# Kernel tuning notes

Hardware: AMD Instinct MI355X
Metric: run time of the kernel (lower is better)

The kernel has to match this reference:

```python
import jax, jax.numpy as jnp
import numpy as np

BN_EPS = 1e-3


def _three_nn(unknown, known):
    # unknown: [B, N2, 3] query points; known: [B, N1, 3]
    # returns squared distances and indices of the 3 nearest known points
    # (CUDA three_nn returns squared euclidean distances).
    d2 = (jnp.sum(unknown * unknown, -1)[:, :, None]
          + jnp.sum(known * known, -1)[:, None, :]
          - 2.0 * jnp.einsum('bnd,bmd->bnm', unknown, known))  # [B, N2, N1]
    neg_top, ind = jax.lax.top_k(-d2, 3)                        # [B, N2, 3]
    dist2 = jnp.maximum(-neg_top, 0.0)
    return dist2, ind


def _conv_bn_relu(x, W, b, gamma, beta, mean, var):
    # x: [B, C_in, N]; W: [C_out, C_in] (1x1 conv); inference-mode BN
    y = jnp.einsum('oc,bcn->bon', W, x) + b[None, :, None]
    scale = gamma / jnp.sqrt(var + BN_EPS)
    y = (y - mean[None, :, None]) * scale[None, :, None] + beta[None, :, None]
    return jax.nn.relu(y)


def setup_inputs() -> dict:
    key = jax.random.key(0)
    ks = jax.random.split(key, 12)
    B, N1, N2, C1, C2, H = 2, 4096, 16384, 256, 128, 256
    return {
        'points1': jax.random.normal(ks[0], (B, 3, N1), jnp.float32),
        'points2': jax.random.normal(ks[1], (B, 3, N2), jnp.float32),
        'features1': jax.random.normal(ks[2], (B, C1, N1), jnp.float32),
        'features2': jax.random.normal(ks[3], (B, C2, N2), jnp.float32),
        'W1': jax.random.normal(ks[4], (H, C1 + C2), jnp.float32) * 0.05,
        'b1': jax.random.normal(ks[5], (H,), jnp.float32) * 0.05,
        'gamma1': jnp.ones((H,), jnp.float32),
        'beta1': jnp.zeros((H,), jnp.float32),
        'mean1': jax.random.normal(ks[6], (H,), jnp.float32) * 0.1,
        'var1': jax.random.uniform(ks[7], (H,), jnp.float32, 0.5, 1.5),
        'W2': jax.random.normal(ks[8], (H, H), jnp.float32) * 0.05,
        'b2': jax.random.normal(ks[9], (H,), jnp.float32) * 0.05,
        'gamma2': jnp.ones((H,), jnp.float32),
        'beta2': jnp.zeros((H,), jnp.float32),
        'mean2': jax.random.normal(ks[10], (H,), jnp.float32) * 0.1,
        'var2': jax.random.uniform(ks[11], (H,), jnp.float32, 0.5, 1.5),
    }


def reference(points1, points2, features1, features2,
              W1, b1, gamma1, beta1, mean1, var1,
              W2, b2, gamma2, beta2, mean2, var2):
    # 3-NN of each dense point (points2) among coarse points (points1)
    unknown = jnp.swapaxes(points2, 1, 2)  # [B, N2, 3]
    known = jnp.swapaxes(points1, 1, 2)    # [B, N1, 3]
    dist, ind = _three_nn(unknown, known)  # dist: squared distances [B, N2, 3]
    dist = dist * dist                     # forward squares again (as in source)
    dist = jnp.maximum(dist, 1e-10)
    inv = 1.0 / dist
    weights = inv / jnp.sum(inv, axis=2, keepdims=True)  # [B, N2, 3]

    # gather features of the 3 neighbors: features1 [B, C1, N1] -> [B, N2, 3, C1]
    f1 = jnp.swapaxes(features1, 1, 2)  # [B, N1, C1]
    gathered = jax.vmap(lambda f, i: f[i])(f1, ind)  # [B, N2, 3, C1]
    interp = jnp.einsum('bnkc,bnk->bcn', gathered, weights)  # [B, C1, N2]

    x = jnp.concatenate([interp, features2], axis=1)  # [B, C1+C2, N2]
    x = _conv_bn_relu(x, W1, b1, gamma1, beta1, mean1, var1)
    x = _conv_bn_relu(x, W2, b2, gamma2, beta2, mean2, var2)
    return x
```

## Files before the change

### kernel.cpp

```cpp
#include <hip/hip_runtime.h>
#include <cstdint>
#include <cstddef>

#define N1 4096
#define N2 16384
#define C1 256
#define C2 128
#define HH 256
#define K1 384
#define BQ 32768
#define KPAD 392
#define NCH 8

typedef float  f32x4  __attribute__((ext_vector_type(4)));
typedef __bf16 bf16x8 __attribute__((ext_vector_type(8)));
typedef __bf16 bf16x4 __attribute__((ext_vector_type(4)));

__device__ __forceinline__ float exact_dd(float ux, float uy, float uz,
                                          float su, float4 p) {
  float dot = __fadd_rn(__fadd_rn(__fmul_rn(ux, p.x), __fmul_rn(uy, p.y)),
                        __fmul_rn(uz, p.z));
  return __builtin_fmaf(dot, -2.0f, __fadd_rn(su, p.w));
}

#define LEXINS(da, db, dc, ia, ib, ic, dd, jj)                                 \
  {                                                                            \
    bool ca = ((dd) < (da)) || ((dd) == (da) && (jj) < (ia));                  \
    bool cb = ((dd) < (db)) || ((dd) == (db) && (jj) < (ib));                  \
    bool cc = ((dd) < (dc)) || ((dd) == (dc) && (jj) < (ic));                  \
    dc = cb ? (db) : (cc ? (dd) : (dc));                                       \
    ic = cb ? (ib) : (cc ? (jj) : (ic));                                       \
    db = ca ? (da) : (cb ? (dd) : (db));                                       \
    ib = ca ? (ia) : (cb ? (jj) : (ib));                                       \
    da = ca ? (dd) : (da);                                                     \
    ia = ca ? (jj) : (ia);                                                     \
  }

#define KMIN4(K1_, K2_, K3_, K4_, x)                                           \
  {                                                                            \
    float n1 = fminf((K1_), (x));                                              \
    float n2 = __builtin_amdgcn_fmed3f((K1_), (x), (K2_));                     \
    float n3 = __builtin_amdgcn_fmed3f((K2_), (x), (K3_));                     \
    float n4 = __builtin_amdgcn_fmed3f((K3_), (x), (K4_));                     \
    K1_ = n1; K2_ = n2; K3_ = n3; K4_ = n4;                                    \
  }

#define POINTQ(ux, uy, uz, su, px, py, pz, pw, jj, Ka, Kb, Kc, Kd)             \
  {                                                                            \
    float dot_ = __fadd_rn(                                                    \
        __fadd_rn(__fmul_rn((ux), (px)), __fmul_rn((uy), (py))),               \
        __fmul_rn((uz), (pz)));                                                \
    float dd_ = __builtin_fmaf(dot_, -2.0f, __fadd_rn((su), (pw)));            \
    float xk_ = __uint_as_float((__float_as_uint(dd_) & 0xFFFFF000u) |         \
                                ((unsigned)(jj) & 0x00000FFFu));               \
    KMIN4(Ka, Kb, Kc, Kd, xk_);                                                \
  }

__global__ __launch_bounds__(256) void k_prep(
    const float* __restrict__ p1,
    const float* __restrict__ W1, const float* __restrict__ W2,
    const float* __restrict__ b1, const float* __restrict__ g1,
    const float* __restrict__ be1, const float* __restrict__ mm1,
    const float* __restrict__ vv1,
    const float* __restrict__ b2, const float* __restrict__ g2,
    const float* __restrict__ be2, const float* __restrict__ mm2,
    const float* __restrict__ vv2,
    float4* __restrict__ pts4,
    __bf16* __restrict__ W1b, __bf16* __restrict__ W2b,
    float* __restrict__ scsh) {
  int idx = blockIdx.x * 256 + threadIdx.x;
  if (idx < HH * K1) W1b[idx] = (__bf16)W1[idx];
  if (idx < HH * HH) W2b[idx] = (__bf16)W2[idx];
  if (idx < 2 * N1) {
    int b = idx >> 12, j = idx & (N1 - 1);
    const float* p = p1 + (size_t)b * 3 * N1;
    float x = p[j], y = p[N1 + j], z = p[2 * N1 + j];
    float sk = __fadd_rn(__fadd_rn(__fmul_rn(x, x), __fmul_rn(y, y)),
                         __fmul_rn(z, z));
    pts4[idx] = make_float4(x, y, z, sk);
  }
  if (idx < HH) {
    float sc = g1[idx] / sqrtf(vv1[idx] + 1e-3f);
    scsh[idx]          = sc;
    scsh[HH + idx]     = fmaf(b1[idx] - mm1[idx], sc, be1[idx]);
    float s2 = g2[idx] / sqrtf(vv2[idx] + 1e-3f);
    scsh[2 * HH + idx] = s2;
    scsh[3 * HH + idx] = fmaf(b2[idx] - mm2[idx], s2, be2[idx]);
  }
}

__global__ __launch_bounds__(256) void k_nn(
    const float* __restrict__ p2, const float4* __restrict__ pts4,
    float* __restrict__ keybuf) {
#pragma clang fp contract(off)
  __shared__ float4 spts[512];
  const int bx = blockIdx.x;
  const int ch = bx & (NCH - 1);
  const int qt = bx >> 3;
  const int b  = qt >> 5;
  const int nA = ((qt & 31) << 9) + threadIdx.x;
  const int nB = nA + 256;

  {
    const float4* g = pts4 + (size_t)b * N1 + ch * 512;
    spts[threadIdx.x]       = g[threadIdx.x];
    spts[threadIdx.x + 256] = g[threadIdx.x + 256];
  }

  const float* p2b = p2 + (size_t)b * 3 * N2;
  float uxA = p2b[nA], uyA = p2b[N2 + nA], uzA = p2b[2 * N2 + nA];
  float suA = __fadd_rn(__fadd_rn(__fmul_rn(uxA, uxA), __fmul_rn(uyA, uyA)),
                        __fmul_rn(uzA, uzA));
  float uxB = p2b[nB], uyB = p2b[N2 + nB], uzB = p2b[2 * N2 + nB];
  float suB = __fadd_rn(__fadd_rn(__fmul_rn(uxB, uxB), __fmul_rn(uyB, uyB)),
                        __fmul_rn(uzB, uzB));
  __syncthreads();

  const int j0 = ch * 512;
  float KaA = 3.0e38f, KbA = 3.0e38f, KcA = 3.0e38f, KdA = 3.0e38f;
  float KaB = 3.0e38f, KbB = 3.0e38f, KcB = 3.0e38f, KdB = 3.0e38f;
#pragma unroll 4
  for (int k = 0; k < 256; ++k) {
    float4 p0 = spts[2 * k];
    float4 p1 = spts[2 * k + 1];
    int i0 = j0 + 2 * k;
    int i1 = j0 + 2 * k + 1;
    POINTQ(uxA, uyA, uzA, suA, p0.x, p0.y, p0.z, p0.w, i0, KaA, KbA, KcA, KdA);
    POINTQ(uxA, uyA, uzA, suA, p1.x, p1.y, p1.z, p1.w, i1, KaA, KbA, KcA, KdA);
    POINTQ(uxB, uyB, uzB, suB, p0.x, p0.y, p0.z, p0.w, i0, KaB, KbB, KcB, KdB);
    POINTQ(uxB, uyB, uzB, suB, p1.x, p1.y, p1.z, p1.w, i1, KaB, KbB, KcB, KdB);
  }

  int qA = b * N2 + nA;
  int qB = b * N2 + nB;
  keybuf[(ch * 4 + 0) * BQ + qA] = KaA;
  keybuf[(ch * 4 + 1) * BQ + qA] = KbA;
  keybuf[(ch * 4 + 2) * BQ + qA] = KcA;
  keybuf[(ch * 4 + 3) * BQ + qA] = KdA;
  keybuf[(ch * 4 + 0) * BQ + qB] = KaB;
  keybuf[(ch * 4 + 1) * BQ + qB] = KbB;
  keybuf[(ch * 4 + 2) * BQ + qB] = KcB;
  keybuf[(ch * 4 + 3) * BQ + qB] = KdB;
}

__global__ __launch_bounds__(256) void k_merge(
    const float* __restrict__ keybuf, const float4* __restrict__ pts4,
    const float* __restrict__ p2,
    float* __restrict__ wbuf, int* __restrict__ ibuf) {
#pragma clang fp contract(off)
  int tid = blockIdx.x * 256 + threadIdx.x;
  int sub = tid & 3;
  int q = tid >> 2;
  int b = q >> 14, n = q & (N2 - 1);

  const float* p2b = p2 + (size_t)b * 3 * N2;
  float ux = p2b[n], uy = p2b[N2 + n], uz = p2b[2 * N2 + n];
  float su = __fadd_rn(__fadd_rn(__fmul_rn(ux, ux), __fmul_rn(uy, uy)),
                       __fmul_rn(uz, uz));

  float Ka = 3.0e38f, Kb = 3.0e38f, Kc = 3.0e38f, Kd = 3.0e38f;
#pragma unroll 4
  for (int m = 0; m < 8; ++m) {
    float x = keybuf[(sub * 8 + m) * BQ + q];
    KMIN4(Ka, Kb, Kc, Kd, x);
  }
#pragma unroll
  for (int msk = 1; msk <= 2; msk <<= 1) {
    float ea = __shfl_xor(Ka, msk, 64), eb = __shfl_xor(Kb, msk, 64);
    float ec = __shfl_xor(Kc, msk, 64), ed = __shfl_xor(Kd, msk, 64);
    KMIN4(Ka, Kb, Kc, Kd, ea);
    KMIN4(Ka, Kb, Kc, Kd, eb);
    KMIN4(Ka, Kb, Kc, Kd, ec);
    KMIN4(Ka, Kb, Kc, Kd, ed);
  }
  if (sub != 0) return;

  bool flag = (__float_as_uint(Kc) >> 12) == (__float_as_uint(Kd) >> 12);
  const float4* pb = pts4 + (size_t)b * N1;
  float da, db, dc;
  int ia, ib, ic;
  if (!flag) {
    ia = (int)(__float_as_uint(Ka) & 0xFFFu);
    ib = (int)(__float_as_uint(Kb) & 0xFFFu);
    ic = (int)(__float_as_uint(Kc) & 0xFFFu);
    da = exact_dd(ux, uy, uz, su, pb[ia]);
    db = exact_dd(ux, uy, uz, su, pb[ib]);
    dc = exact_dd(ux, uy, uz, su, pb[ic]);
  } else {
    da = 3.0e38f; db = 3.0e38f; dc = 3.0e38f;
    ia = 0x7fffffff; ib = 0x7fffffff; ic = 0x7fffffff;
    for (int i = 0; i < 4 * NCH; ++i) {
      float x = keybuf[i * BQ + q];
      int jj = (int)(__float_as_uint(x) & 0xFFFu);
      float dd = exact_dd(ux, uy, uz, su, pb[jj]);
      LEXINS(da, db, dc, ia, ib, ic, dd, jj);
    }
  }

  float qa = fmaxf(da, 0.0f), qb = fmaxf(db, 0.0f), qc = fmaxf(dc, 0.0f);
  qa = fmaxf(__fmul_rn(qa, qa), 1e-10f);
  qb = fmaxf(__fmul_rn(qb, qb), 1e-10f);
  qc = fmaxf(__fmul_rn(qc, qc), 1e-10f);
  float va = __fdiv_rn(1.0f, qa);
  float vb = __fdiv_rn(1.0f, qb);
  float vc = __fdiv_rn(1.0f, qc);
  float s = __fadd_rn(__fadd_rn(va, vb), vc);
  wbuf[q]           = __fdiv_rn(va, s);
  wbuf[BQ + q]      = __fdiv_rn(vb, s);
  wbuf[2 * BQ + q]  = __fdiv_rn(vc, s);
  ibuf[q]          = ia;
  ibuf[BQ + q]     = ib;
  ibuf[2 * BQ + q] = ic;
}

__global__ __launch_bounds__(256) void k_transpose(
    const float* __restrict__ f1, float* __restrict__ f1T) {
  __shared__ float tile[64][65];
  const int bx = blockIdx.x;
  const int b = bx >> 8;
  const int rest = bx & 255;
  const int ct = rest >> 6;
  const int ntb = (rest & 63) << 6;
  const int t = threadIdx.x;
  const int ln = t & 63, g = t >> 6;

  const float* src = f1 + ((size_t)b * C1 + ct * 64) * N1 + ntb;
  for (int k = 0; k < 16; ++k) {
    int c = (k << 2) + g;
    tile[c][ln] = src[(size_t)c * N1 + ln];
  }
  __syncthreads();
  float* dst = f1T + ((size_t)b * N1 + ntb) * C1 + ct * 64;
  for (int k = 0; k < 16; ++k) {
    int nn = (k << 2) + g;
    dst[(size_t)nn * C1 + ln] = tile[ln][nn];
  }
}

__global__ __launch_bounds__(512) void k_fused(
    const float* __restrict__ f1T, const float* __restrict__ f2,
    const float* __restrict__ wbuf, const int* __restrict__ ibuf,
    const __bf16* __restrict__ W1b, const __bf16* __restrict__ W2b,
    const float* __restrict__ scsh, float* __restrict__ out) {
  __shared__ __bf16 sX[64 * KPAD];
  const int t = threadIdx.x;
  const int bx = blockIdx.x;
  const int b = bx >> 8;
  const int n0 = (bx & 255) << 6;

  {
    const int nn = t >> 3, qq = t & 7;
    const int gi = b * N2 + n0 + nn;
    const float w0 = wbuf[gi], w1 = wbuf[BQ + gi], w2 = wbuf[2 * BQ + gi];
    const int i0 = ibuf[gi], i1 = ibuf[BQ + gi], i2 = ibuf[2 * BQ + gi];
    const float4* r0 = (const float4*)(f1T + ((size_t)b * N1 + i0) * C1);
    const float4* r1 = (const float4*)(f1T + ((size_t)b * N1 + i1) * C1);
    const float4* r2 = (const float4*)(f1T + ((size_t)b * N1 + i2) * C1);
#pragma unroll 4
    for (int m = 0; m < 8; ++m) {
      int idx4 = (qq << 3) + m;
      float4 a = r0[idx4], c4 = r1[idx4], d4 = r2[idx4];
      bf16x4 v;
      v[0] = (__bf16)fmaf(w0, a.x, fmaf(w1, c4.x, w2 * d4.x));
      v[1] = (__bf16)fmaf(w0, a.y, fmaf(w1, c4.y, w2 * d4.y));
      v[2] = (__bf16)fmaf(w0, a.z, fmaf(w1, c4.z, w2 * d4.z));
      v[3] = (__bf16)fmaf(w0, a.w, fmaf(w1, c4.w, w2 * d4.w));
      *(bf16x4*)&sX[nn * KPAD + (idx4 << 2)] = v;
    }
  }
  {
    const int col = t & 63, g = t >> 6;
    const float* f2b = f2 + (size_t)b * C2 * N2 + n0 + col;
#pragma unroll
    for (int m = 0; m < 4; ++m) {
      int c4 = (g << 4) + (m << 2);
      bf16x4 v;
      v[0] = (__bf16)f2b[(size_t)(c4 + 0) * N2];
      v[1] = (__bf16)f2b[(size_t)(c4 + 1) * N2];
      v[2] = (__bf16)f2b[(size_t)(c4 + 2) * N2];
      v[3] = (__bf16)f2b[(size_t)(c4 + 3) * N2];
      *(bf16x4*)&sX[col * KPAD + 256 + c4] = v;
    }
  }
  __syncthreads();

  const int l  = t & 63;
  const int wv = __builtin_amdgcn_readfirstlane(t >> 6);
  const int ob = wv << 5;
  const int lm = l & 15, lg = l >> 4;

  f32x4 acc[2][4];
#pragma unroll
  for (int mt = 0; mt < 2; ++mt)
#pragma unroll
    for (int nt = 0; nt < 4; ++nt) acc[mt][nt] = (f32x4)0.0f;

  for (int ks = 0; ks < 12; ++ks) {
    bf16x8 af[2], bfr[4];
#pragma unroll
    for (int mt = 0; mt < 2; ++mt)
      af[mt] = *(const bf16x8*)(W1b + (size_t)(ob + mt * 16 + lm) * K1 +
                                ks * 32 + lg * 8);
#pragma unroll
    for (int nt = 0; nt < 4; ++nt)
      bfr[nt] = *(const bf16x8*)&sX[(nt * 16 + lm) * KPAD + ks * 32 + lg * 8];
#pragma unroll
    for (int mt = 0; mt < 2; ++mt)
#pragma unroll
      for (int nt = 0; nt < 4; ++nt)
        acc[mt][nt] = __builtin_amdgcn_mfma_f32_16x16x32_bf16(
            af[mt], bfr[nt], acc[mt][nt], 0, 0, 0);
  }
  __syncthreads();

#pragma unroll
  for (int mt = 0; mt < 2; ++mt) {
    int rb = ob + mt * 16 + lg * 4;
    float4 sc4 = *(const float4*)(scsh + rb);
    float4 sh4 = *(const float4*)(scsh + HH + rb);
#pragma unroll
    for (int nt = 0; nt < 4; ++nt) {
      int colc = nt * 16 + lm;
      bf16x4 v;
      v[0] = (__bf16)fmaxf(fmaf(acc[mt][nt][0], sc4.x, sh4.x), 0.0f);
      v[1] = (__bf16)fmaxf(fmaf(acc[mt][nt][1], sc4.y, sh4.y), 0.0f);
      v[2] = (__bf16)fmaxf(fmaf(acc[mt][nt][2], sc4.z, sh4.z), 0.0f);
      v[3] = (__bf16)fmaxf(fmaf(acc[mt][nt][3], sc4.w, sh4.w), 0.0f);
      *(bf16x4*)&sX[colc * KPAD + rb] = v;
    }
  }
  __syncthreads();

  f32x4 ac2[2][4];
#pragma unroll
  for (int mt = 0; mt < 2; ++mt)
#pragma unroll
    for (int nt = 0; nt < 4; ++nt) ac2[mt][nt] = (f32x4)0.0f;
  for (int ks = 0; ks < 8; ++ks) {
    bf16x8 af[2], bfr[4];
#pragma unroll
    for (int mt = 0; mt < 2; ++mt)
      af[mt] = *(const bf16x8*)(W2b + (size_t)(ob + mt * 16 + lm) * HH +
                                ks * 32 + lg * 8);
#pragma unroll
    for (int nt = 0; nt < 4; ++nt)
      bfr[nt] = *(const bf16x8*)&sX[(nt * 16 + lm) * KPAD + ks * 32 + lg * 8];
#pragma unroll
    for (int mt = 0; mt < 2; ++mt)
#pragma unroll
      for (int nt = 0; nt < 4; ++nt)
        ac2[mt][nt] = __builtin_amdgcn_mfma_f32_16x16x32_bf16(
            af[mt], bfr[nt], ac2[mt][nt], 0, 0, 0);
  }

  float* outb = out + (size_t)b * HH * N2 + n0;
#pragma unroll
  for (int mt = 0; mt < 2; ++mt) {
    int rb = ob + mt * 16 + lg * 4;
    float4 sc4 = *(const float4*)(scsh + 2 * HH + rb);
    float4 sh4 = *(const float4*)(scsh + 3 * HH + rb);
#pragma unroll
    for (int nt = 0; nt < 4; ++nt) {
      int colc = nt * 16 + lm;
      outb[(size_t)(rb + 0) * N2 + colc] =
          fmaxf(fmaf(ac2[mt][nt][0], sc4.x, sh4.x), 0.0f);
      outb[(size_t)(rb + 1) * N2 + colc] =
          fmaxf(fmaf(ac2[mt][nt][1], sc4.y, sh4.y), 0.0f);
      outb[(size_t)(rb + 2) * N2 + colc] =
          fmaxf(fmaf(ac2[mt][nt][2], sc4.z, sh4.z), 0.0f);
      outb[(size_t)(rb + 3) * N2 + colc] =
          fmaxf(fmaf(ac2[mt][nt][3], sc4.w, sh4.w), 0.0f);
    }
  }
}

extern "C" void kernel_launch(void* const* d_in, const int* in_sizes, int n_in,
                              void* d_out, int out_size, void* d_ws, size_t ws_size,
                              hipStream_t stream) {
  const float* p1  = (const float*)d_in[0];
  const float* p2  = (const float*)d_in[1];
  const float* f1  = (const float*)d_in[2];
  const float* f2  = (const float*)d_in[3];
  const float* W1  = (const float*)d_in[4];
  const float* bb1 = (const float*)d_in[5];
  const float* g1  = (const float*)d_in[6];
  const float* be1 = (const float*)d_in[7];
  const float* mm1 = (const float*)d_in[8];
  const float* vv1 = (const float*)d_in[9];
  const float* W2  = (const float*)d_in[10];
  const float* bb2 = (const float*)d_in[11];
  const float* g2  = (const float*)d_in[12];
  const float* be2 = (const float*)d_in[13];
  const float* mm2 = (const float*)d_in[14];
  const float* vv2 = (const float*)d_in[15];
  float* out = (float*)d_out;

  char* ws = (char*)d_ws;
  float*  keybuf = (float*)(ws);
  float*  f1T    = (float*)(ws);
  float*  wbuf   = (float*)(ws + 8388608);
  int*    ibuf   = (int*)  (ws + 8781824);
  float4* pts4   = (float4*)(ws + 9306112);
  __bf16* W1b    = (__bf16*)(ws + 9437184);
  __bf16* W2b    = (__bf16*)(ws + 9633792);
  float*  scsh   = (float*)(ws + 9764864);

  k_prep<<<384, 256, 0, stream>>>(p1, W1, W2,
                                  bb1, g1, be1, mm1, vv1,
                                  bb2, g2, be2, mm2, vv2,
                                  pts4, W1b, W2b, scsh);
  k_nn<<<512, 256, 0, stream>>>(p2, pts4, keybuf);
  k_merge<<<512, 256, 0, stream>>>(keybuf, pts4, p2, wbuf, ibuf);
  k_transpose<<<512, 256, 0, stream>>>(f1, f1T);
  k_fused<<<512, 512, 0, stream>>>(f1T, f2, wbuf, ibuf, W1b, W2b, scsh, out);
}
```

Baseline: 113.1 us.

## Merge prep, transpose and kNN kernels into one heterogeneous front kernel

```diff
diff --git a/kernel.cpp b/kernel.cpp
--- a/kernel.cpp
+++ b/kernel.cpp
@@ -21,6 +21,14 @@
   float dot = __fadd_rn(__fadd_rn(__fmul_rn(ux, p.x), __fmul_rn(uy, p.y)),
                         __fmul_rn(uz, p.z));
   return __builtin_fmaf(dot, -2.0f, __fadd_rn(su, p.w));
+}
+
+__device__ __forceinline__ float4 load_pt(const float* __restrict__ p1b,
+                                          int j) {
+  float x = p1b[j], y = p1b[N1 + j], z = p1b[2 * N1 + j];
+  float sk = __fadd_rn(__fadd_rn(__fmul_rn(x, x), __fmul_rn(y, y)),
+                       __fmul_rn(z, z));
+  return make_float4(x, y, z, sk);
 }
 
 #define LEXINS(da, db, dc, ia, ib, ic, dd, jj)                                 \
@@ -56,8 +64,9 @@
     KMIN4(Ka, Kb, Kc, Kd, xk_);                                                \
   }
 
-__global__ __launch_bounds__(256) void k_prep(
-    const float* __restrict__ p1,
+__global__ __launch_bounds__(256) void k_front(
+    const float* __restrict__ p1, const float* __restrict__ p2,
+    const float* __restrict__ f1,
     const float* __restrict__ W1, const float* __restrict__ W2,
     const float* __restrict__ b1, const float* __restrict__ g1,
     const float* __restrict__ be1, const float* __restrict__ mm1,
@@ -65,46 +74,65 @@
     const float* __restrict__ b2, const float* __restrict__ g2,
     const float* __restrict__ be2, const float* __restrict__ mm2,
     const float* __restrict__ vv2,
-    float4* __restrict__ pts4,
     __bf16* __restrict__ W1b, __bf16* __restrict__ W2b,
-    float* __restrict__ scsh) {
-  int idx = blockIdx.x * 256 + threadIdx.x;
-  if (idx < HH * K1) W1b[idx] = (__bf16)W1[idx];
-  if (idx < HH * HH) W2b[idx] = (__bf16)W2[idx];
-  if (idx < 2 * N1) {
-    int b = idx >> 12, j = idx & (N1 - 1);
-    const float* p = p1 + (size_t)b * 3 * N1;
-    float x = p[j], y = p[N1 + j], z = p[2 * N1 + j];
-    float sk = __fadd_rn(__fadd_rn(__fmul_rn(x, x), __fmul_rn(y, y)),
-                         __fmul_rn(z, z));
-    pts4[idx] = make_float4(x, y, z, sk);
-  }
-  if (idx < HH) {
-    float sc = g1[idx] / sqrtf(vv1[idx] + 1e-3f);
-    scsh[idx]          = sc;
-    scsh[HH + idx]     = fmaf(b1[idx] - mm1[idx], sc, be1[idx]);
-    float s2 = g2[idx] / sqrtf(vv2[idx] + 1e-3f);
-    scsh[2 * HH + idx] = s2;
-    scsh[3 * HH + idx] = fmaf(b2[idx] - mm2[idx], s2, be2[idx]);
-  }
-}
-
-__global__ __launch_bounds__(256) void k_nn(
-    const float* __restrict__ p2, const float4* __restrict__ pts4,
+    float* __restrict__ scsh, float* __restrict__ f1T,
     float* __restrict__ keybuf) {
 #pragma clang fp contract(off)
-  __shared__ float4 spts[512];
+  __shared__ __align__(16) float smemf[64 * 65];
   const int bx = blockIdx.x;
-  const int ch = bx & (NCH - 1);
-  const int qt = bx >> 3;
+  const int t = threadIdx.x;
+
+  if (bx < 384) {
+    int idx = bx * 256 + t;
+    if (idx < HH * K1) W1b[idx] = (__bf16)W1[idx];
+    if (idx < HH * HH) W2b[idx] = (__bf16)W2[idx];
+    if (idx < HH) {
+      float sc = g1[idx] / sqrtf(vv1[idx] + 1e-3f);
+      scsh[idx]          = sc;
+      scsh[HH + idx]     = fmaf(b1[idx] - mm1[idx], sc, be1[idx]);
+      float s2 = g2[idx] / sqrtf(vv2[idx] + 1e-3f);
+      scsh[2 * HH + idx] = s2;
+      scsh[3 * HH + idx] = fmaf(b2[idx] - mm2[idx], s2, be2[idx]);
+    }
+    return;
+  }
+
+  if (bx < 896) {
+    float (*tile)[65] = (float(*)[65])smemf;
+    const int bz = bx - 384;
+    const int b = bz >> 8;
+    const int rest = bz & 255;
+    const int ct = rest >> 6;
+    const int ntb = (rest & 63) << 6;
+    const int ln = t & 63, g = t >> 6;
+
+    const float* src = f1 + ((size_t)b * C1 + ct * 64) * N1 + ntb;
+    for (int k = 0; k < 16; ++k) {
+      int c = (k << 2) + g;
+      tile[c][ln] = src[(size_t)c * N1 + ln];
+    }
+    __syncthreads();
+    float* dst = f1T + ((size_t)b * N1 + ntb) * C1 + ct * 64;
+    for (int k = 0; k < 16; ++k) {
+      int nn = (k << 2) + g;
+      dst[(size_t)nn * C1 + ln] = tile[ln][nn];
+    }
+    return;
+  }
+
+  float4* spts = (float4*)smemf;
+  const int bz = bx - 896;
+  const int ch = bz & (NCH - 1);
+  const int qt = bz >> 3;
   const int b  = qt >> 5;
-  const int nA = ((qt & 31) << 9) + threadIdx.x;
+  const int nA = ((qt & 31) << 9) + t;
   const int nB = nA + 256;
 
+  const float* p1b = p1 + (size_t)b * 3 * N1;
   {
-    const float4* g = pts4 + (size_t)b * N1 + ch * 512;
-    spts[threadIdx.x]       = g[threadIdx.x];
-    spts[threadIdx.x + 256] = g[threadIdx.x + 256];
+    int j = ch * 512 + t;
+    spts[t]       = load_pt(p1b, j);
+    spts[t + 256] = load_pt(p1b, j + 256);
   }
 
   const float* p2b = p2 + (size_t)b * 3 * N2;
@@ -122,13 +150,13 @@
 #pragma unroll 4
   for (int k = 0; k < 256; ++k) {
     float4 p0 = spts[2 * k];
-    float4 p1 = spts[2 * k + 1];
+    float4 p1v = spts[2 * k + 1];
     int i0 = j0 + 2 * k;
     int i1 = j0 + 2 * k + 1;
     POINTQ(uxA, uyA, uzA, suA, p0.x, p0.y, p0.z, p0.w, i0, KaA, KbA, KcA, KdA);
-    POINTQ(uxA, uyA, uzA, suA, p1.x, p1.y, p1.z, p1.w, i1, KaA, KbA, KcA, KdA);
+    POINTQ(uxA, uyA, uzA, suA, p1v.x, p1v.y, p1v.z, p1v.w, i1, KaA, KbA, KcA, KdA);
     POINTQ(uxB, uyB, uzB, suB, p0.x, p0.y, p0.z, p0.w, i0, KaB, KbB, KcB, KdB);
-    POINTQ(uxB, uyB, uzB, suB, p1.x, p1.y, p1.z, p1.w, i1, KaB, KbB, KcB, KdB);
+    POINTQ(uxB, uyB, uzB, suB, p1v.x, p1v.y, p1v.z, p1v.w, i1, KaB, KbB, KcB, KdB);
   }
 
   int qA = b * N2 + nA;
@@ -144,7 +172,7 @@
 }
 
 __global__ __launch_bounds__(256) void k_merge(
-    const float* __restrict__ keybuf, const float4* __restrict__ pts4,
+    const float* __restrict__ keybuf, const float* __restrict__ p1,
     const float* __restrict__ p2,
     float* __restrict__ wbuf, int* __restrict__ ibuf) {
 #pragma clang fp contract(off)
@@ -176,23 +204,23 @@
   if (sub != 0) return;
 
   bool flag = (__float_as_uint(Kc) >> 12) == (__float_as_uint(Kd) >> 12);
-  const float4* pb = pts4 + (size_t)b * N1;
+  const float* p1b = p1 + (size_t)b * 3 * N1;
   float da, db, dc;
   int ia, ib, ic;
   if (!flag) {
     ia = (int)(__float_as_uint(Ka) & 0xFFFu);
     ib = (int)(__float_as_uint(Kb) & 0xFFFu);
     ic = (int)(__float_as_uint(Kc) & 0xFFFu);
-    da = exact_dd(ux, uy, uz, su, pb[ia]);
-    db = exact_dd(ux, uy, uz, su, pb[ib]);
-    dc = exact_dd(ux, uy, uz, su, pb[ic]);
+    da = exact_dd(ux, uy, uz, su, load_pt(p1b, ia));
+    db = exact_dd(ux, uy, uz, su, load_pt(p1b, ib));
+    dc = exact_dd(ux, uy, uz, su, load_pt(p1b, ic));
   } else {
     da = 3.0e38f; db = 3.0e38f; dc = 3.0e38f;
     ia = 0x7fffffff; ib = 0x7fffffff; ic = 0x7fffffff;
     for (int i = 0; i < 4 * NCH; ++i) {
       float x = keybuf[i * BQ + q];
       int jj = (int)(__float_as_uint(x) & 0xFFFu);
-      float dd = exact_dd(ux, uy, uz, su, pb[jj]);
+      float dd = exact_dd(ux, uy, uz, su, load_pt(p1b, jj));
       LEXINS(da, db, dc, ia, ib, ic, dd, jj);
     }
   }
@@ -211,30 +239,6 @@
   ibuf[q]          = ia;
   ibuf[BQ + q]     = ib;
   ibuf[2 * BQ + q] = ic;
-}
-
-__global__ __launch_bounds__(256) void k_transpose(
-    const float* __restrict__ f1, float* __restrict__ f1T) {
-  __shared__ float tile[64][65];
-  const int bx = blockIdx.x;
-  const int b = bx >> 8;
-  const int rest = bx & 255;
-  const int ct = rest >> 6;
-  const int ntb = (rest & 63) << 6;
-  const int t = threadIdx.x;
-  const int ln = t & 63, g = t >> 6;
-
-  const float* src = f1 + ((size_t)b * C1 + ct * 64) * N1 + ntb;
-  for (int k = 0; k < 16; ++k) {
-    int c = (k << 2) + g;
-    tile[c][ln] = src[(size_t)c * N1 + ln];
-  }
-  __syncthreads();
-  float* dst = f1T + ((size_t)b * N1 + ntb) * C1 + ct * 64;
-  for (int k = 0; k < 16; ++k) {
-    int nn = (k << 2) + g;
-    dst[(size_t)nn * C1 + ln] = tile[ln][nn];
-  }
 }
 
 __global__ __launch_bounds__(512) void k_fused(
@@ -396,21 +400,18 @@
   float* out = (float*)d_out;
 
   char* ws = (char*)d_ws;
-  float*  keybuf = (float*)(ws);
   float*  f1T    = (float*)(ws);
-  float*  wbuf   = (float*)(ws + 8388608);
-  int*    ibuf   = (int*)  (ws + 8781824);
-  float4* pts4   = (float4*)(ws + 9306112);
-  __bf16* W1b    = (__bf16*)(ws + 9437184);
-  __bf16* W2b    = (__bf16*)(ws + 9633792);
-  float*  scsh   = (float*)(ws + 9764864);
-
-  k_prep<<<384, 256, 0, stream>>>(p1, W1, W2,
-                                  bb1, g1, be1, mm1, vv1,
-                                  bb2, g2, be2, mm2, vv2,
-                                  pts4, W1b, W2b, scsh);
-  k_nn<<<512, 256, 0, stream>>>(p2, pts4, keybuf);
-  k_merge<<<512, 256, 0, stream>>>(keybuf, pts4, p2, wbuf, ibuf);
-  k_transpose<<<512, 256, 0, stream>>>(f1, f1T);
+  float*  keybuf = (float*)(ws + 8388608);
+  float*  wbuf   = (float*)(ws + 12582912);
+  int*    ibuf   = (int*)  (ws + 12976128);
+  __bf16* W1b    = (__bf16*)(ws + 13369344);
+  __bf16* W2b    = (__bf16*)(ws + 13565952);
+  float*  scsh   = (float*)(ws + 13697024);
+
+  k_front<<<1408, 256, 0, stream>>>(p1, p2, f1, W1, W2,
+                                    bb1, g1, be1, mm1, vv1,
+                                    bb2, g2, be2, mm2, vv2,
+                                    W1b, W2b, scsh, f1T, keybuf);
+  k_merge<<<512, 256, 0, stream>>>(keybuf, p1, p2, wbuf, ibuf);
   k_fused<<<512, 512, 0, stream>>>(f1T, f2, wbuf, ibuf, W1b, W2b, scsh, out);
 }
```

New measurement: 106.4 us. 6.0% less time.
